# Optimization experiments

Measured on AMD Instinct MI355X. Metric: run time of the kernel, lower is better.

The kernel has to match this reference:

```python
import jax, jax.numpy as jnp
import numpy as np

B, H, W, DIM, HEADS = 8, 128, 128, 256, 8
LH, LW = 8, 8
HD = DIM // HEADS
SCALE = HD ** -0.5
WS = LH * LW  # window size (tokens per window)


def setup_inputs() -> dict:
    key = jax.random.key(0)
    k1, k2, k3 = jax.random.split(key, 3)
    qkv = jax.random.normal(k1, (3, B, H * W, DIM), jnp.float32)
    lepe_w = jax.random.normal(k2, (DIM, 1, 3, 3), jnp.float32) * 0.1  # depthwise conv weight
    lepe_b = jax.random.normal(k3, (DIM,), jnp.float32) * 0.1
    return {"qkv": qkv, "lepe_w": lepe_w, "lepe_b": lepe_b}


def _to_local(x):
    # [B, L, C] -> [B*nH*nW, heads, LH*LW, head_dim]  (window partition)
    Bb, L, C = x.shape
    x = x.reshape(Bb, H // LH, LH, W // LW, LW, C).transpose(0, 1, 3, 2, 4, 5)
    x = x.reshape(-1, WS, HEADS, HD).transpose(0, 2, 1, 3)
    return x


def reference(qkv, lepe_w, lepe_b):
    q, k, v = qkv[0], qkv[1], qkv[2]
    Bb, L, C = q.shape
    q = _to_local(q) * SCALE            # [nWin, h, ws, d]
    k = _to_local(k)                    # [nWin, h, ws, d]
    # v windows in NCHW for depthwise LePE conv: [nWin, C, LH, LW]
    vw = v.reshape(Bb, H // LH, LH, W // LW, LW, C).transpose(0, 1, 3, 5, 2, 4)
    vw = vw.reshape(-1, C, LH, LW)
    lepe = jax.lax.conv_general_dilated(
        vw, lepe_w, window_strides=(1, 1), padding='SAME',
        feature_group_count=C,
        dimension_numbers=('NCHW', 'OIHW', 'NCHW')) + lepe_b[None, :, None, None]
    lepe = lepe.reshape(-1, HEADS, HD, WS).transpose(0, 1, 3, 2)   # [nWin, h, ws, d]
    vloc = vw.reshape(-1, HEADS, HD, WS).transpose(0, 1, 3, 2)     # [nWin, h, ws, d]
    attn = jax.nn.softmax(jnp.einsum('whqd,whkd->whqk', q, k), axis=-1)
    x = jnp.einsum('whqk,whkd->whqd', attn, vloc) + lepe           # [nWin, h, ws, d]
    # window merge back to [B, L, C]
    x = x.transpose(0, 2, 1, 3).reshape(-1, WS, C)
    x = x.reshape(Bb, H // LH, W // LW, LH, LW, C).transpose(0, 1, 3, 2, 4, 5)
    x = x.reshape(Bb, H * W, C)
    return x, q
```

## Files before the change

kernel.cpp:

```cpp
#include <hip/hip_runtime.h>


#define SCALE_F 0.17677669529663687f

typedef __attribute__((ext_vector_type(8))) short bf16x8;
typedef __attribute__((ext_vector_type(4))) float f32x4;
typedef __attribute__((ext_vector_type(4))) unsigned int u32x4;

static __device__ __forceinline__ unsigned short f2bf(float f) {
    unsigned u = __builtin_bit_cast(unsigned, f);
    u += 0x7fffu + ((u >> 16) & 1u);
    return (unsigned short)(u >> 16);
}
static __device__ __forceinline__ float bf2f_lo(unsigned u) {
    return __builtin_bit_cast(float, u << 16);
}
static __device__ __forceinline__ float bf2f_hi(unsigned u) {
    return __builtin_bit_cast(float, u & 0xffff0000u);
}

__global__ __launch_bounds__(256, 6) void lepe_attn_kernel(
    const float* __restrict__ qkv,
    const float* __restrict__ lw,
    const float* __restrict__ lb,
    float* __restrict__ out)
{
    const int bid  = blockIdx.x;
    const int head = bid & 7;
    const int win  = bid >> 3;
    const int ww   = win & 15;
    const int wh   = (win >> 4) & 15;
    const int b    = win >> 8;
    const int t    = threadIdx.x;

    __shared__ __align__(16) short q_s[64][40];
    __shared__ __align__(16) short k_s[64][40];
    __shared__ __align__(16) short v_t[32][72];
    __shared__ __align__(16) unsigned v_pair[64][18];
    __shared__ float w_s[288];
    __shared__ float b_s[32];

    const float* Qp = qkv;
    const float* Kp = qkv + (size_t)33554432;
    const float* Vp = qkv + (size_t)67108864;
    float* xout = out;
    float* qout = out + (size_t)33554432;

    for (int i = t; i < 288; i += 256) w_s[i] = lw[head * 288 + i];
    if (t < 32) b_s[t] = lb[head * 32 + t];

    #pragma unroll
    for (int u = 0; u < 2; ++u) {
        const int idx = t + u * 256;
        const int s   = idx >> 3;
        const int d4  = idx & 7;
        const int row = wh * 8 + (s >> 3);
        const int col = ww * 8 + (s & 7);
        const size_t goff = ((size_t)(b * 16384 + row * 128 + col)) * 256
                          + head * 32 + d4 * 4;

        float4 fq = *(const float4*)(Qp + goff);
        float4 fk = *(const float4*)(Kp + goff);
        float4 fv = *(const float4*)(Vp + goff);

        fq.x *= SCALE_F; fq.y *= SCALE_F; fq.z *= SCALE_F; fq.w *= SCALE_F;
        *(float4*)(qout + ((size_t)bid * 64 + s) * 32 + d4 * 4) = fq;

        uint2 qp, kp;
        qp.x = (unsigned)f2bf(fq.x) | ((unsigned)f2bf(fq.y) << 16);
        qp.y = (unsigned)f2bf(fq.z) | ((unsigned)f2bf(fq.w) << 16);
        kp.x = (unsigned)f2bf(fk.x) | ((unsigned)f2bf(fk.y) << 16);
        kp.y = (unsigned)f2bf(fk.z) | ((unsigned)f2bf(fk.w) << 16);
        *(uint2*)&q_s[s][d4 * 4] = qp;
        *(uint2*)&k_s[s][d4 * 4] = kp;

        const unsigned short b0 = f2bf(fv.x), b1 = f2bf(fv.y),
                             b2 = f2bf(fv.z), b3 = f2bf(fv.w);
        const int sp = ((s >> 1) & 1) * 32 + ((s >> 2) & 3) * 8
                     + (s & 1) * 4 + (s >> 4);
        v_t[d4 * 4 + 0][sp] = (short)b0;
        v_t[d4 * 4 + 1][sp] = (short)b1;
        v_t[d4 * 4 + 2][sp] = (short)b2;
        v_t[d4 * 4 + 3][sp] = (short)b3;
        const unsigned short vb[4] = {b0, b1, b2, b3};
        #pragma unroll
        for (int j = 0; j < 4; ++j) {
            const int ch = d4 * 4 + j;
            ((unsigned short*)&v_pair[s][ch & 15])[ch >> 4] = vb[j];
        }
    }
    __syncthreads();

    const int lane = t & 63;
    const int wid  = t >> 6;
    const int c    = lane & 15;
    const int g    = lane >> 4;
    const int i0   = wid * 16;

    const bf16x8 bq = *(const bf16x8*)&q_s[i0 + c][g * 8];
    f32x4 sacc[4];
    #pragma unroll
    for (int jt = 0; jt < 4; ++jt) {
        const bf16x8 ak = *(const bf16x8*)&k_s[jt * 16 + c][g * 8];
        f32x4 acc = {0.f, 0.f, 0.f, 0.f};
        sacc[jt] = __builtin_amdgcn_mfma_f32_16x16x32_bf16(ak, bq, acc, 0, 0, 0);
    }

    float mx = -3.0e38f;
    #pragma unroll
    for (int jt = 0; jt < 4; ++jt)
        #pragma unroll
        for (int r = 0; r < 4; ++r)
            mx = fmaxf(mx, sacc[jt][r]);
    mx = fmaxf(mx, __shfl_xor(mx, 16));
    mx = fmaxf(mx, __shfl_xor(mx, 32));

    float p[4][4];
    float sm = 0.f;
    #pragma unroll
    for (int jt = 0; jt < 4; ++jt)
        #pragma unroll
        for (int r = 0; r < 4; ++r) {
            p[jt][r] = __expf(sacc[jt][r] - mx);
            sm += p[jt][r];
        }
    sm += __shfl_xor(sm, 16);
    sm += __shfl_xor(sm, 32);
    const float inv = 1.0f / sm;

    unsigned dwA[4], dwB[4];
    #pragma unroll
    for (int r = 0; r < 4; ++r) {
        dwA[r] = (unsigned)f2bf(p[0][r] * inv)
               | ((unsigned)f2bf(p[1][r] * inv) << 16);
        dwB[r] = (unsigned)f2bf(p[2][r] * inv)
               | ((unsigned)f2bf(p[3][r] * inv) << 16);
    }
    const u32x4 w0 = {dwA[0], dwB[0], dwA[1], dwB[1]};
    const u32x4 w1 = {dwA[2], dwB[2], dwA[3], dwB[3]};
    const bf16x8 pa0 = __builtin_bit_cast(bf16x8, w0);
    const bf16x8 pa1 = __builtin_bit_cast(bf16x8, w1);

    f32x4 o0 = {0.f, 0.f, 0.f, 0.f};
    f32x4 o1 = {0.f, 0.f, 0.f, 0.f};
    {
        const bf16x8 vb00 = *(const bf16x8*)&v_t[c][g * 8];
        const bf16x8 vb10 = *(const bf16x8*)&v_t[16 + c][g * 8];
        const bf16x8 vb01 = *(const bf16x8*)&v_t[c][32 + g * 8];
        const bf16x8 vb11 = *(const bf16x8*)&v_t[16 + c][32 + g * 8];
        o0 = __builtin_amdgcn_mfma_f32_16x16x32_bf16(pa0, vb00, o0, 0, 0, 0);
        o1 = __builtin_amdgcn_mfma_f32_16x16x32_bf16(pa0, vb10, o1, 0, 0, 0);
        o0 = __builtin_amdgcn_mfma_f32_16x16x32_bf16(pa1, vb01, o0, 0, 0, 0);
        o1 = __builtin_amdgcn_mfma_f32_16x16x32_bf16(pa1, vb11, o1, 0, 0, 0);
    }

    const int srow  = 2 * wid + (g >> 1);
    const int scol0 = 4 * (g & 1);

    unsigned pr[3][6];
    #pragma unroll
    for (int dy = 0; dy < 3; ++dy) {
        const int rr   = srow + dy - 1;
        const bool rok = (rr >= 0) && (rr < 8);
        const int rcl  = rok ? rr : 0;
        #pragma unroll
        for (int dx = 0; dx < 6; ++dx) {
            const int cc   = scol0 + dx - 1;
            const bool cok = (cc >= 0) && (cc < 8);
            const int ccl  = cok ? cc : 0;
            const unsigned val = v_pair[rcl * 8 + ccl][c];
            pr[dy][dx] = (rok && cok) ? val : 0u;
        }
    }
    #pragma unroll
    for (int half = 0; half < 2; ++half) {
        const int ch = c + 16 * half;
        float wv[9];
        #pragma unroll
        for (int k2 = 0; k2 < 9; ++k2) wv[k2] = w_s[ch * 9 + k2];
        float acc[4] = {b_s[ch], b_s[ch], b_s[ch], b_s[ch]};
        #pragma unroll
        for (int dy = 0; dy < 3; ++dy) {
            float rowv[6];
            #pragma unroll
            for (int dx = 0; dx < 6; ++dx)
                rowv[dx] = half ? bf2f_hi(pr[dy][dx]) : bf2f_lo(pr[dy][dx]);
            #pragma unroll
            for (int r = 0; r < 4; ++r)
                #pragma unroll
                for (int dk = 0; dk < 3; ++dk)
                    acc[r] += wv[dy * 3 + dk] * rowv[r + dk];
        }
        #pragma unroll
        for (int r = 0; r < 4; ++r) {
            if (half == 0) o0[r] += acc[r]; else o1[r] += acc[r];
        }
    }

    #pragma unroll
    for (int r = 0; r < 4; ++r) {
        const int s   = i0 + 4 * g + r;
        const int row = wh * 8 + (s >> 3);
        const int col = ww * 8 + (s & 7);
        float* xo = xout + ((size_t)(b * 16384 + row * 128 + col)) * 256
                  + head * 32;
        xo[c]      = o0[r];
        xo[16 + c] = o1[r];
    }
}

extern "C" void kernel_launch(void* const* d_in, const int* in_sizes, int n_in,
                              void* d_out, int out_size, void* d_ws, size_t ws_size,
                              hipStream_t stream) {
    (void)in_sizes; (void)n_in; (void)out_size; (void)d_ws; (void)ws_size;
    const float* qkv = (const float*)d_in[0];
    const float* lw  = (const float*)d_in[1];
    const float* lb  = (const float*)d_in[2];
    float* out = (float*)d_out;
    lepe_attn_kernel<<<dim3(16384), dim3(256), 0, stream>>>(qkv, lw, lb, out);
}
```

Baseline: 145.9 us.

## Load Q/K fragments directly from global into MFMA registers, bypassing LDS

Each lane now reads its Q and K fragments straight from global memory in the layout the MFMA expects. The q_s and k_s shared buffers and their staging writes are removed. The QK^T MFMA and the softmax now run before the barrier, which overlaps with the V staging into LDS, and the barrier moves to just before the PV product. K is read four times per block (once per wave) instead of once, which adds global/L2 traffic and register pressure. Launch bounds drop from 6 to 5 waves to make room for the extra registers.

```diff
diff --git a/kernel.cpp b/kernel.cpp
--- a/kernel.cpp
+++ b/kernel.cpp
@@ -12,6 +12,9 @@
     u += 0x7fffu + ((u >> 16) & 1u);
     return (unsigned short)(u >> 16);
 }
+static __device__ __forceinline__ unsigned pack2(float a, float b) {
+    return (unsigned)f2bf(a) | ((unsigned)f2bf(b) << 16);
+}
 static __device__ __forceinline__ float bf2f_lo(unsigned u) {
     return __builtin_bit_cast(float, u << 16);
 }
@@ -19,7 +22,7 @@
     return __builtin_bit_cast(float, u & 0xffff0000u);
 }
 
-__global__ __launch_bounds__(256, 6) void lepe_attn_kernel(
+__global__ __launch_bounds__(256, 5) void lepe_attn_kernel(
     const float* __restrict__ qkv,
     const float* __restrict__ lw,
     const float* __restrict__ lb,
@@ -33,8 +36,6 @@
     const int b    = win >> 8;
     const int t    = threadIdx.x;
 
-    __shared__ __align__(16) short q_s[64][40];
-    __shared__ __align__(16) short k_s[64][40];
     __shared__ __align__(16) short v_t[32][72];
     __shared__ __align__(16) unsigned v_pair[64][18];
     __shared__ float w_s[288];
@@ -46,34 +47,75 @@
     float* xout = out;
     float* qout = out + (size_t)33554432;
 
-    for (int i = t; i < 288; i += 256) w_s[i] = lw[head * 288 + i];
-    if (t < 32) b_s[t] = lb[head * 32 + t];
-
+    const size_t wbase = ((size_t)(b * 16384 + (wh * 8) * 128 + ww * 8)) * 256
+                       + head * 32;
+
+    const int lane = t & 63;
+    const int wid  = t >> 6;
+    const int c    = lane & 15;
+    const int g    = lane >> 4;
+    const int i0   = wid * 16;
+
+    const int sq = i0 + c;
+    const float* qptr = Qp + wbase + ((sq >> 3) * 128 + (sq & 7)) * 256 + g * 8;
+    float4 q0 = *(const float4*)(qptr);
+    float4 q1 = *(const float4*)(qptr + 4);
+
+    float4 k0[4], k1[4];
+    #pragma unroll
+    for (int jt = 0; jt < 4; ++jt) {
+        const int sk = jt * 16 + c;
+        const float* kptr = Kp + wbase
+                          + ((sk >> 3) * 128 + (sk & 7)) * 256 + g * 8;
+        k0[jt] = *(const float4*)(kptr);
+        k1[jt] = *(const float4*)(kptr + 4);
+    }
+
+    float4 v04[2];
     #pragma unroll
     for (int u = 0; u < 2; ++u) {
         const int idx = t + u * 256;
         const int s   = idx >> 3;
         const int d4  = idx & 7;
-        const int row = wh * 8 + (s >> 3);
-        const int col = ww * 8 + (s & 7);
-        const size_t goff = ((size_t)(b * 16384 + row * 128 + col)) * 256
-                          + head * 32 + d4 * 4;
-
-        float4 fq = *(const float4*)(Qp + goff);
-        float4 fk = *(const float4*)(Kp + goff);
-        float4 fv = *(const float4*)(Vp + goff);
-
-        fq.x *= SCALE_F; fq.y *= SCALE_F; fq.z *= SCALE_F; fq.w *= SCALE_F;
-        *(float4*)(qout + ((size_t)bid * 64 + s) * 32 + d4 * 4) = fq;
-
-        uint2 qp, kp;
-        qp.x = (unsigned)f2bf(fq.x) | ((unsigned)f2bf(fq.y) << 16);
-        qp.y = (unsigned)f2bf(fq.z) | ((unsigned)f2bf(fq.w) << 16);
-        kp.x = (unsigned)f2bf(fk.x) | ((unsigned)f2bf(fk.y) << 16);
-        kp.y = (unsigned)f2bf(fk.z) | ((unsigned)f2bf(fk.w) << 16);
-        *(uint2*)&q_s[s][d4 * 4] = qp;
-        *(uint2*)&k_s[s][d4 * 4] = kp;
-
+        v04[u] = *(const float4*)(Vp + wbase
+                 + ((s >> 3) * 128 + (s & 7)) * 256 + d4 * 4);
+    }
+
+    for (int i = t; i < 288; i += 256) w_s[i] = lw[head * 288 + i];
+    if (t < 32) b_s[t] = lb[head * 32 + t];
+
+    q0.x *= SCALE_F; q0.y *= SCALE_F; q0.z *= SCALE_F; q0.w *= SCALE_F;
+    q1.x *= SCALE_F; q1.y *= SCALE_F; q1.z *= SCALE_F; q1.w *= SCALE_F;
+    {
+        float* qo = qout + ((size_t)bid * 64 + sq) * 32 + g * 8;
+        *(float4*)(qo)     = q0;
+        *(float4*)(qo + 4) = q1;
+    }
+    const u32x4 qw = {pack2(q0.x, q0.y), pack2(q0.z, q0.w),
+                      pack2(q1.x, q1.y), pack2(q1.z, q1.w)};
+    const bf16x8 bq = __builtin_bit_cast(bf16x8, qw);
+
+    bf16x8 ak[4];
+    #pragma unroll
+    for (int jt = 0; jt < 4; ++jt) {
+        const u32x4 kw = {pack2(k0[jt].x, k0[jt].y), pack2(k0[jt].z, k0[jt].w),
+                          pack2(k1[jt].x, k1[jt].y), pack2(k1[jt].z, k1[jt].w)};
+        ak[jt] = __builtin_bit_cast(bf16x8, kw);
+    }
+
+    f32x4 sacc[4];
+    #pragma unroll
+    for (int jt = 0; jt < 4; ++jt) {
+        f32x4 acc = {0.f, 0.f, 0.f, 0.f};
+        sacc[jt] = __builtin_amdgcn_mfma_f32_16x16x32_bf16(ak[jt], bq, acc, 0, 0, 0);
+    }
+
+    #pragma unroll
+    for (int u = 0; u < 2; ++u) {
+        const int idx = t + u * 256;
+        const int s   = idx >> 3;
+        const int d4  = idx & 7;
+        const float4 fv = v04[u];
         const unsigned short b0 = f2bf(fv.x), b1 = f2bf(fv.y),
                              b2 = f2bf(fv.z), b3 = f2bf(fv.w);
         const int sp = ((s >> 1) & 1) * 32 + ((s >> 2) & 3) * 8
@@ -89,22 +131,6 @@
             ((unsigned short*)&v_pair[s][ch & 15])[ch >> 4] = vb[j];
         }
     }
-    __syncthreads();
-
-    const int lane = t & 63;
-    const int wid  = t >> 6;
-    const int c    = lane & 15;
-    const int g    = lane >> 4;
-    const int i0   = wid * 16;
-
-    const bf16x8 bq = *(const bf16x8*)&q_s[i0 + c][g * 8];
-    f32x4 sacc[4];
-    #pragma unroll
-    for (int jt = 0; jt < 4; ++jt) {
-        const bf16x8 ak = *(const bf16x8*)&k_s[jt * 16 + c][g * 8];
-        f32x4 acc = {0.f, 0.f, 0.f, 0.f};
-        sacc[jt] = __builtin_amdgcn_mfma_f32_16x16x32_bf16(ak, bq, acc, 0, 0, 0);
-    }
 
     float mx = -3.0e38f;
     #pragma unroll
@@ -131,15 +157,15 @@
     unsigned dwA[4], dwB[4];
     #pragma unroll
     for (int r = 0; r < 4; ++r) {
-        dwA[r] = (unsigned)f2bf(p[0][r] * inv)
-               | ((unsigned)f2bf(p[1][r] * inv) << 16);
-        dwB[r] = (unsigned)f2bf(p[2][r] * inv)
-               | ((unsigned)f2bf(p[3][r] * inv) << 16);
+        dwA[r] = pack2(p[0][r] * inv, p[1][r] * inv);
+        dwB[r] = pack2(p[2][r] * inv, p[3][r] * inv);
     }
     const u32x4 w0 = {dwA[0], dwB[0], dwA[1], dwB[1]};
     const u32x4 w1 = {dwA[2], dwB[2], dwA[3], dwB[3]};
     const bf16x8 pa0 = __builtin_bit_cast(bf16x8, w0);
     const bf16x8 pa1 = __builtin_bit_cast(bf16x8, w1);
+
+    __syncthreads();
 
     f32x4 o0 = {0.f, 0.f, 0.f, 0.f};
     f32x4 o1 = {0.f, 0.f, 0.f, 0.f};
```

Result: slower. 170.9 us (+17.1%).

## Process four windows per block with register prefetch of next window

Applied to the files above, without the earlier changes.

Each block now loops over four consecutive windows for one head instead of handling a single window, and prefetches the next window's Q/K/V float4 values into registers while computing the current one. The grid shrinks to a quarter, weights and bias load once per block, and global-load latency is meant to overlap with the MFMA, softmax and conv work. The extra prefetch registers lower the occupancy hint from 6 to 5 blocks per CU, and an added barrier per iteration guards reuse of shared memory.

```diff
diff --git a/kernel.cpp b/kernel.cpp
--- a/kernel.cpp
+++ b/kernel.cpp
@@ -2,6 +2,7 @@
 
 
 #define SCALE_F 0.17677669529663687f
+#define PAIRS 4
 
 typedef __attribute__((ext_vector_type(8))) short bf16x8;
 typedef __attribute__((ext_vector_type(4))) float f32x4;
@@ -12,6 +13,9 @@
     u += 0x7fffu + ((u >> 16) & 1u);
     return (unsigned short)(u >> 16);
 }
+static __device__ __forceinline__ unsigned pack2(float a, float b) {
+    return (unsigned)f2bf(a) | ((unsigned)f2bf(b) << 16);
+}
 static __device__ __forceinline__ float bf2f_lo(unsigned u) {
     return __builtin_bit_cast(float, u << 16);
 }
@@ -19,18 +23,14 @@
     return __builtin_bit_cast(float, u & 0xffff0000u);
 }
 
-__global__ __launch_bounds__(256, 6) void lepe_attn_kernel(
+__global__ __launch_bounds__(256, 5) void lepe_attn_kernel(
     const float* __restrict__ qkv,
     const float* __restrict__ lw,
     const float* __restrict__ lb,
     float* __restrict__ out)
 {
-    const int bid  = blockIdx.x;
-    const int head = bid & 7;
-    const int win  = bid >> 3;
-    const int ww   = win & 15;
-    const int wh   = (win >> 4) & 15;
-    const int b    = win >> 8;
+    const int head = blockIdx.x & 7;
+    const int wg   = blockIdx.x >> 3;
     const int t    = threadIdx.x;
 
     __shared__ __align__(16) short q_s[64][40];
@@ -49,47 +49,8 @@
     for (int i = t; i < 288; i += 256) w_s[i] = lw[head * 288 + i];
     if (t < 32) b_s[t] = lb[head * 32 + t];
 
-    #pragma unroll
-    for (int u = 0; u < 2; ++u) {
-        const int idx = t + u * 256;
-        const int s   = idx >> 3;
-        const int d4  = idx & 7;
-        const int row = wh * 8 + (s >> 3);
-        const int col = ww * 8 + (s & 7);
-        const size_t goff = ((size_t)(b * 16384 + row * 128 + col)) * 256
-                          + head * 32 + d4 * 4;
-
-        float4 fq = *(const float4*)(Qp + goff);
-        float4 fk = *(const float4*)(Kp + goff);
-        float4 fv = *(const float4*)(Vp + goff);
-
-        fq.x *= SCALE_F; fq.y *= SCALE_F; fq.z *= SCALE_F; fq.w *= SCALE_F;
-        *(float4*)(qout + ((size_t)bid * 64 + s) * 32 + d4 * 4) = fq;
-
-        uint2 qp, kp;
-        qp.x = (unsigned)f2bf(fq.x) | ((unsigned)f2bf(fq.y) << 16);
-        qp.y = (unsigned)f2bf(fq.z) | ((unsigned)f2bf(fq.w) << 16);
-        kp.x = (unsigned)f2bf(fk.x) | ((unsigned)f2bf(fk.y) << 16);
-        kp.y = (unsigned)f2bf(fk.z) | ((unsigned)f2bf(fk.w) << 16);
-        *(uint2*)&q_s[s][d4 * 4] = qp;
-        *(uint2*)&k_s[s][d4 * 4] = kp;
-
-        const unsigned short b0 = f2bf(fv.x), b1 = f2bf(fv.y),
-                             b2 = f2bf(fv.z), b3 = f2bf(fv.w);
-        const int sp = ((s >> 1) & 1) * 32 + ((s >> 2) & 3) * 8
-                     + (s & 1) * 4 + (s >> 4);
-        v_t[d4 * 4 + 0][sp] = (short)b0;
-        v_t[d4 * 4 + 1][sp] = (short)b1;
-        v_t[d4 * 4 + 2][sp] = (short)b2;
-        v_t[d4 * 4 + 3][sp] = (short)b3;
-        const unsigned short vb[4] = {b0, b1, b2, b3};
-        #pragma unroll
-        for (int j = 0; j < 4; ++j) {
-            const int ch = d4 * 4 + j;
-            ((unsigned short*)&v_pair[s][ch & 15])[ch >> 4] = vb[j];
-        }
-    }
-    __syncthreads();
+    const int s0 = t >> 3;
+    const int d4 = t & 7;
 
     const int lane = t & 63;
     const int wid  = t >> 6;
@@ -97,115 +58,194 @@
     const int g    = lane >> 4;
     const int i0   = wid * 16;
 
-    const bf16x8 bq = *(const bf16x8*)&q_s[i0 + c][g * 8];
-    f32x4 sacc[4];
+    auto wbase = [&](int win) -> size_t {
+        const int ww = win & 15;
+        const int wh = (win >> 4) & 15;
+        const int b  = win >> 8;
+        return ((size_t)(b * 16384 + (wh * 8) * 128 + ww * 8)) * 256
+             + head * 32;
+    };
+    auto toff = [&](int s) -> int { return ((s >> 3) * 128 + (s & 7)) * 256; };
+
+    float4 cq[2], ck[2], cv[2];
+    {
+        const size_t base = wbase(wg * PAIRS);
+        #pragma unroll
+        for (int u = 0; u < 2; ++u) {
+            const int s = s0 + 32 * u;
+            const size_t goff = base + toff(s) + d4 * 4;
+            cq[u] = *(const float4*)(Qp + goff);
+            ck[u] = *(const float4*)(Kp + goff);
+            cv[u] = *(const float4*)(Vp + goff);
+        }
+    }
+
     #pragma unroll
-    for (int jt = 0; jt < 4; ++jt) {
-        const bf16x8 ak = *(const bf16x8*)&k_s[jt * 16 + c][g * 8];
-        f32x4 acc = {0.f, 0.f, 0.f, 0.f};
-        sacc[jt] = __builtin_amdgcn_mfma_f32_16x16x32_bf16(ak, bq, acc, 0, 0, 0);
-    }
-
-    float mx = -3.0e38f;
-    #pragma unroll
-    for (int jt = 0; jt < 4; ++jt)
-        #pragma unroll
-        for (int r = 0; r < 4; ++r)
-            mx = fmaxf(mx, sacc[jt][r]);
-    mx = fmaxf(mx, __shfl_xor(mx, 16));
-    mx = fmaxf(mx, __shfl_xor(mx, 32));
-
-    float p[4][4];
-    float sm = 0.f;
-    #pragma unroll
-    for (int jt = 0; jt < 4; ++jt)
+    for (int it = 0; it < PAIRS; ++it) {
+        const int win = wg * PAIRS + it;
+        const int bid = win * 8 + head;
+
+        float4 nq[2], nk[2], nv[2];
+        if (it + 1 < PAIRS) {
+            const size_t base = wbase(win + 1);
+            #pragma unroll
+            for (int u = 0; u < 2; ++u) {
+                const int s = s0 + 32 * u;
+                const size_t goff = base + toff(s) + d4 * 4;
+                nq[u] = *(const float4*)(Qp + goff);
+                nk[u] = *(const float4*)(Kp + goff);
+                nv[u] = *(const float4*)(Vp + goff);
+            }
+        }
+
+        #pragma unroll
+        for (int u = 0; u < 2; ++u) {
+            const int s = s0 + 32 * u;
+            float4 fq = cq[u];
+            fq.x *= SCALE_F; fq.y *= SCALE_F; fq.z *= SCALE_F; fq.w *= SCALE_F;
+            *(float4*)(qout + ((size_t)bid * 64 + s) * 32 + d4 * 4) = fq;
+
+            uint2 qp, kp;
+            qp.x = pack2(fq.x, fq.y);
+            qp.y = pack2(fq.z, fq.w);
+            kp.x = pack2(ck[u].x, ck[u].y);
+            kp.y = pack2(ck[u].z, ck[u].w);
+            *(uint2*)&q_s[s][d4 * 4] = qp;
+            *(uint2*)&k_s[s][d4 * 4] = kp;
+
+            const float4 fv = cv[u];
+            const unsigned short b0 = f2bf(fv.x), b1 = f2bf(fv.y),
+                                 b2 = f2bf(fv.z), b3 = f2bf(fv.w);
+            const int sp = ((s >> 1) & 1) * 32 + ((s >> 2) & 3) * 8
+                         + (s & 1) * 4 + (s >> 4);
+            v_t[d4 * 4 + 0][sp] = (short)b0;
+            v_t[d4 * 4 + 1][sp] = (short)b1;
+            v_t[d4 * 4 + 2][sp] = (short)b2;
+            v_t[d4 * 4 + 3][sp] = (short)b3;
+            const unsigned short vb[4] = {b0, b1, b2, b3};
+            #pragma unroll
+            for (int j = 0; j < 4; ++j) {
+                const int ch = d4 * 4 + j;
+                ((unsigned short*)&v_pair[s][ch & 15])[ch >> 4] = vb[j];
+            }
+        }
+        __syncthreads();
+
+        const bf16x8 bq = *(const bf16x8*)&q_s[i0 + c][g * 8];
+        f32x4 sacc[4];
+        #pragma unroll
+        for (int jt = 0; jt < 4; ++jt) {
+            const bf16x8 ak = *(const bf16x8*)&k_s[jt * 16 + c][g * 8];
+            f32x4 acc = {0.f, 0.f, 0.f, 0.f};
+            sacc[jt] = __builtin_amdgcn_mfma_f32_16x16x32_bf16(ak, bq, acc,
+                                                               0, 0, 0);
+        }
+
+        float mx = -3.0e38f;
+        #pragma unroll
+        for (int jt = 0; jt < 4; ++jt)
+            #pragma unroll
+            for (int r = 0; r < 4; ++r)
+                mx = fmaxf(mx, sacc[jt][r]);
+        mx = fmaxf(mx, __shfl_xor(mx, 16));
+        mx = fmaxf(mx, __shfl_xor(mx, 32));
+
+        float p[4][4];
+        float sm = 0.f;
+        #pragma unroll
+        for (int jt = 0; jt < 4; ++jt)
+            #pragma unroll
+            for (int r = 0; r < 4; ++r) {
+                p[jt][r] = __expf(sacc[jt][r] - mx);
+                sm += p[jt][r];
+            }
+        sm += __shfl_xor(sm, 16);
+        sm += __shfl_xor(sm, 32);
+        const float inv = 1.0f / sm;
+
+        unsigned dwA[4], dwB[4];
         #pragma unroll
         for (int r = 0; r < 4; ++r) {
-            p[jt][r] = __expf(sacc[jt][r] - mx);
-            sm += p[jt][r];
-        }
-    sm += __shfl_xor(sm, 16);
-    sm += __shfl_xor(sm, 32);
-    const float inv = 1.0f / sm;
-
-    unsigned dwA[4], dwB[4];
-    #pragma unroll
-    for (int r = 0; r < 4; ++r) {
-        dwA[r] = (unsigned)f2bf(p[0][r] * inv)
-               | ((unsigned)f2bf(p[1][r] * inv) << 16);
-        dwB[r] = (unsigned)f2bf(p[2][r] * inv)
-               | ((unsigned)f2bf(p[3][r] * inv) << 16);
-    }
-    const u32x4 w0 = {dwA[0], dwB[0], dwA[1], dwB[1]};
-    const u32x4 w1 = {dwA[2], dwB[2], dwA[3], dwB[3]};
-    const bf16x8 pa0 = __builtin_bit_cast(bf16x8, w0);
-    const bf16x8 pa1 = __builtin_bit_cast(bf16x8, w1);
-
-    f32x4 o0 = {0.f, 0.f, 0.f, 0.f};
-    f32x4 o1 = {0.f, 0.f, 0.f, 0.f};
-    {
-        const bf16x8 vb00 = *(const bf16x8*)&v_t[c][g * 8];
-        const bf16x8 vb10 = *(const bf16x8*)&v_t[16 + c][g * 8];
-        const bf16x8 vb01 = *(const bf16x8*)&v_t[c][32 + g * 8];
-        const bf16x8 vb11 = *(const bf16x8*)&v_t[16 + c][32 + g * 8];
-        o0 = __builtin_amdgcn_mfma_f32_16x16x32_bf16(pa0, vb00, o0, 0, 0, 0);
-        o1 = __builtin_amdgcn_mfma_f32_16x16x32_bf16(pa0, vb10, o1, 0, 0, 0);
-        o0 = __builtin_amdgcn_mfma_f32_16x16x32_bf16(pa1, vb01, o0, 0, 0, 0);
-        o1 = __builtin_amdgcn_mfma_f32_16x16x32_bf16(pa1, vb11, o1, 0, 0, 0);
-    }
-
-    const int srow  = 2 * wid + (g >> 1);
-    const int scol0 = 4 * (g & 1);
-
-    unsigned pr[3][6];
-    #pragma unroll
-    for (int dy = 0; dy < 3; ++dy) {
-        const int rr   = srow + dy - 1;
-        const bool rok = (rr >= 0) && (rr < 8);
-        const int rcl  = rok ? rr : 0;
-        #pragma unroll
-        for (int dx = 0; dx < 6; ++dx) {
-            const int cc   = scol0 + dx - 1;
-            const bool cok = (cc >= 0) && (cc < 8);
-            const int ccl  = cok ? cc : 0;
-            const unsigned val = v_pair[rcl * 8 + ccl][c];
-            pr[dy][dx] = (rok && cok) ? val : 0u;
-        }
-    }
-    #pragma unroll
-    for (int half = 0; half < 2; ++half) {
-        const int ch = c + 16 * half;
-        float wv[9];
-        #pragma unroll
-        for (int k2 = 0; k2 < 9; ++k2) wv[k2] = w_s[ch * 9 + k2];
-        float acc[4] = {b_s[ch], b_s[ch], b_s[ch], b_s[ch]};
+            dwA[r] = pack2(p[0][r] * inv, p[1][r] * inv);
+            dwB[r] = pack2(p[2][r] * inv, p[3][r] * inv);
+        }
+        const u32x4 w0 = {dwA[0], dwB[0], dwA[1], dwB[1]};
+        const u32x4 w1 = {dwA[2], dwB[2], dwA[3], dwB[3]};
+        const bf16x8 pa0 = __builtin_bit_cast(bf16x8, w0);
+        const bf16x8 pa1 = __builtin_bit_cast(bf16x8, w1);
+
+        f32x4 o0 = {0.f, 0.f, 0.f, 0.f};
+        f32x4 o1 = {0.f, 0.f, 0.f, 0.f};
+        {
+            const bf16x8 vb00 = *(const bf16x8*)&v_t[c][g * 8];
+            const bf16x8 vb10 = *(const bf16x8*)&v_t[16 + c][g * 8];
+            const bf16x8 vb01 = *(const bf16x8*)&v_t[c][32 + g * 8];
+            const bf16x8 vb11 = *(const bf16x8*)&v_t[16 + c][32 + g * 8];
+            o0 = __builtin_amdgcn_mfma_f32_16x16x32_bf16(pa0, vb00, o0, 0, 0, 0);
+            o1 = __builtin_amdgcn_mfma_f32_16x16x32_bf16(pa0, vb10, o1, 0, 0, 0);
+            o0 = __builtin_amdgcn_mfma_f32_16x16x32_bf16(pa1, vb01, o0, 0, 0, 0);
+            o1 = __builtin_amdgcn_mfma_f32_16x16x32_bf16(pa1, vb11, o1, 0, 0, 0);
+        }
+
+        const int srow  = 2 * wid + (g >> 1);
+        const int scol0 = 4 * (g & 1);
+
+        unsigned pr[3][6];
         #pragma unroll
         for (int dy = 0; dy < 3; ++dy) {
-            float rowv[6];
-            #pragma unroll
-            for (int dx = 0; dx < 6; ++dx)
-                rowv[dx] = half ? bf2f_hi(pr[dy][dx]) : bf2f_lo(pr[dy][dx]);
-            #pragma unroll
-            for (int r = 0; r < 4; ++r)
+            const int rr   = srow + dy - 1;
+            const bool rok = (rr >= 0) && (rr < 8);
+            const int rcl  = rok ? rr : 0;
+            #pragma unroll
+            for (int dx = 0; dx < 6; ++dx) {
+                const int cc   = scol0 + dx - 1;
+                const bool cok = (cc >= 0) && (cc < 8);
+                const int ccl  = cok ? cc : 0;
+                const unsigned val = v_pair[rcl * 8 + ccl][c];
+                pr[dy][dx] = (rok && cok) ? val : 0u;
+            }
+        }
+        #pragma unroll
+        for (int half = 0; half < 2; ++half) {
+            const int ch = c + 16 * half;
+            float wv[9];
+            #pragma unroll
+            for (int k2 = 0; k2 < 9; ++k2) wv[k2] = w_s[ch * 9 + k2];
+            float acc[4] = {b_s[ch], b_s[ch], b_s[ch], b_s[ch]};
+            #pragma unroll
+            for (int dy = 0; dy < 3; ++dy) {
+                float rowv[6];
                 #pragma unroll
-                for (int dk = 0; dk < 3; ++dk)
-                    acc[r] += wv[dy * 3 + dk] * rowv[r + dk];
-        }
+                for (int dx = 0; dx < 6; ++dx)
+                    rowv[dx] = half ? bf2f_hi(pr[dy][dx]) : bf2f_lo(pr[dy][dx]);
+                #pragma unroll
+                for (int r = 0; r < 4; ++r)
+                    #pragma unroll
+                    for (int dk = 0; dk < 3; ++dk)
+                        acc[r] += wv[dy * 3 + dk] * rowv[r + dk];
+            }
+            #pragma unroll
+            for (int r = 0; r < 4; ++r) {
+                if (half == 0) o0[r] += acc[r]; else o1[r] += acc[r];
+            }
+        }
+
+        const size_t xbase = wbase(win);
         #pragma unroll
         for (int r = 0; r < 4; ++r) {
-            if (half == 0) o0[r] += acc[r]; else o1[r] += acc[r];
-        }
-    }
-
-    #pragma unroll
-    for (int r = 0; r < 4; ++r) {
-        const int s   = i0 + 4 * g + r;
-        const int row = wh * 8 + (s >> 3);
-        const int col = ww * 8 + (s & 7);
-        float* xo = xout + ((size_t)(b * 16384 + row * 128 + col)) * 256
-                  + head * 32;
-        xo[c]      = o0[r];
-        xo[16 + c] = o1[r];
+            const int s = i0 + 4 * g + r;
+            float* xo = xout + xbase + toff(s);
+            xo[c]      = o0[r];
+            xo[16 + c] = o1[r];
+        }
+
+        if (it + 1 < PAIRS) {
+            __syncthreads();
+            #pragma unroll
+            for (int u = 0; u < 2; ++u) {
+                cq[u] = nq[u]; ck[u] = nk[u]; cv[u] = nv[u];
+            }
+        }
     }
 }
 
@@ -217,5 +257,5 @@
     const float* lw  = (const float*)d_in[1];
     const float* lb  = (const float*)d_in[2];
     float* out = (float*)d_out;
-    lepe_attn_kernel<<<dim3(16384), dim3(256), 0, stream>>>(qkv, lw, lb, out);
-}
+    lepe_attn_kernel<<<dim3(4096), dim3(256), 0, stream>>>(qkv, lw, lb, out);
+}
```

New measurement: 169.1 us. 15.9% more time.
